# Kernel tuning notes

Hardware: AMD Instinct MI355X
Metric: run time of the kernel (lower is better)

Reference implementation:

```python
import jax, jax.numpy as jnp
import numpy as np

R = 12            # search_radius
P = 2 * R + 1     # 25x25 search window
DIV = 512.0       # self.div_num; T = DIV**-0.5


def _relu_l2norm(x, axis=1, eps=1e-12):
    # matches F.relu followed by F.normalize(p=2, dim=1)
    x = jax.nn.relu(x)
    n = jnp.sqrt(jnp.sum(x * x, axis=axis, keepdims=True))
    return x / jnp.maximum(n, eps)


def setup_inputs() -> dict:
    key = jax.random.key(0)
    k1, k2 = jax.random.split(key)
    feat1_video = jax.random.normal(k1, (8, 512, 4, 30, 30), dtype=jnp.float32)  # r50_feat1 (pre relu/norm)
    feat2_img = jax.random.normal(k2, (8, 512, 30, 30), dtype=jnp.float32)       # img_feat2 (pre relu/norm)
    return {"feat1_video": feat1_video, "feat2_img": feat2_img}


def reference(feat1_video, feat2_img):
    # relu + channel L2-normalize, as in forward() before compute_corr_softmax
    video = _relu_l2norm(feat1_video)          # [B,C,T,H,W]  -> r50_feat2 arg
    patch = _relu_l2norm(feat2_img)            # [B,C,H,W]    -> patch_feat1 arg
    B, C, T, H, W = video.shape

    vpad = jnp.pad(video, ((0, 0), (0, 0), (0, 0), (R, R), (R, R)))

    # all 625 (dh, dw) window offsets, vmapped into one fused correlation
    offsets = jnp.stack(
        jnp.meshgrid(jnp.arange(P), jnp.arange(P), indexing="ij"), axis=-1
    ).reshape(-1, 2)  # [P*P, 2]

    def shift_corr(off):
        win = jax.lax.dynamic_slice(
            vpad, (0, 0, 0, off[0], off[1]), (B, C, T, H, W)
        )
        return jnp.einsum("bcthw,bchw->bthw", win, patch)

    corr = jax.vmap(shift_corr)(offsets)               # [P*P, B, T, H, W]
    corr = jnp.transpose(corr, (1, 2, 0, 3, 4))        # [B, T, P*P, H, W]

    # torch: div by div_num**-0.5, then softmax(corr / T) with T = div_num**-0.5
    Tparam = DIV ** (-0.5)
    corr = corr / (DIV ** (-0.5)) / Tparam             # == corr * 512
    sm = jax.nn.softmax(corr, axis=2)

    # validity mask: output pixel y with shift h=dh-R is valid iff 0 <= y+h < H
    dh = jnp.arange(P)
    ys = jnp.arange(H)
    xs = jnp.arange(W)
    valid_h = ((ys[None, :] + dh[:, None] - R) >= 0) & ((ys[None, :] + dh[:, None] - R) < H)  # [P,H]
    valid_w = ((xs[None, :] + dh[:, None] - R) >= 0) & ((xs[None, :] + dh[:, None] - R) < W)  # [P,W]
    valid = valid_h[:, None, :, None] & valid_w[None, :, None, :]  # [P,P,H,W]
    valid = valid.reshape(P * P, H, W)

    out = jnp.where(valid[None, None], sm, jnp.float32(-1.0))      # [B,T,P*P,H,W]
    return out.reshape(B, T, P, P, H, W)
```

## Files before the change

kernel.cpp:

```cpp
#include <hip/hip_runtime.h>

#define RR 12
#define PD 25
#define PP 625
#define HH 30
#define WW 30
#define HWD 900
#define CD 512
#define BD 8
#define TD 4
#define CSTRIDE 628
#define ROWPKB 32768
#define QSCALE 16129.0f
#define EXPK (512.0f / QSCALE)

typedef __attribute__((ext_vector_type(4))) int i32x4;
typedef __attribute__((ext_vector_type(16))) int i32x16;

__global__ __launch_bounds__(256) void norm_pack_kernel(const float* __restrict__ inP,
                                                        const float* __restrict__ inV,
                                                        unsigned char* __restrict__ outA,
                                                        unsigned char* __restrict__ outB) {
    int row = blockIdx.x;
    int plane = blockIdx.y;
    const float* in;
    size_t base;
    int c_stride;
    unsigned char* ob;
    if (plane < 8) {
        in = inP; c_stride = HWD;
        base = (size_t)plane * CD * HWD + row * WW;
        ob = outA + (size_t)(plane * 30 + row) * ROWPKB;
    } else {
        int bt = plane - 8;
        int b = bt >> 2, t = bt & 3;
        in = inV; c_stride = TD * HWD;
        base = (size_t)b * CD * (TD * HWD) + (size_t)t * HWD + row * WW;
        ob = outB + (size_t)(bt * 30 + row) * ROWPKB;
    }
    __shared__ float tile[30][516];
    __shared__ float inv[30];
    int tid = threadIdx.x;
    for (int it = 0; it < 64; ++it) {
        int lin = it * 256 + tid;
        int c = lin >> 5, p = lin & 31;
        if (p < 30) tile[p][c] = fmaxf(in[base + (size_t)c * c_stride + p], 0.f);
    }
    __syncthreads();
    if ((tid >> 3) < 30) {
        int p = tid >> 3, s8 = tid & 7;
        float acc = 0.f;
#pragma unroll
        for (int j = 0; j < 16; ++j) {
            const float4 v = *reinterpret_cast<const float4*>(&tile[p][(s8 + j * 8) * 4]);
            acc += v.x * v.x + v.y * v.y + v.z * v.z + v.w * v.w;
        }
        acc += __shfl_xor(acc, 1);
        acc += __shfl_xor(acc, 2);
        acc += __shfl_xor(acc, 4);
        if (s8 == 0) inv[p] = 1.0f / fmaxf(sqrtf(acc), 1e-12f);
    }
    __syncthreads();
    for (int sl = tid; sl < 1024; sl += 256) {
        int ks = sl >> 6, ln = sl & 63;
        int x = ln & 31;
        if (x > 29) x = 29;
        int kb = ks * 32 + (ln >> 5) * 16;
        float iv = inv[x];
        union { signed char c[16]; i32x4 v; } p1, p2;
#pragma unroll
        for (int j = 0; j < 16; ++j) {
            float nv = tile[x][kb + j] * iv;
            float s1 = rintf(nv * 127.f);
            float r = nv * 127.f - s1;
            float s2 = rintf(r * 254.f);
            p1.c[j] = (signed char)(int)s1;
            p2.c[j] = (signed char)(int)s2;
        }
        *(i32x4*)(ob + (size_t)ks * 2048 + ln * 16) = p1.v;
        *(i32x4*)(ob + (size_t)ks * 2048 + 1024 + ln * 16) = p2.v;
    }
}

__global__ __launch_bounds__(512, 4) void corr_kernel(
    const unsigned char* __restrict__ Apk, const unsigned char* __restrict__ Bpk,
    float* __restrict__ out) {
    int gid = blockIdx.x;
    int r = gid & 7;
    int x_ = gid >> 3;
    int btl = x_ / 30;
    int h = x_ - btl * 30;
    int bt = r * 4 + btl;
    int b = r;

    __shared__ float corr[HH * CSTRIDE];
    __shared__ float is_lds[HH];
    int tid = threadIdx.x;
    int wid = tid >> 6, lane = tid & 63;

    for (int i = tid; i < HH * CSTRIDE; i += 512) corr[i] = 0.f;

    const unsigned char* abase = Apk + (size_t)(b * 30 + h) * ROWPKB + lane * 16;
    const unsigned char* bplane = Bpk + (size_t)bt * 30 * ROWPKB + lane * 16;
    int dh_lo = max(0, RR - h);
    int dh_hi = min(PD - 1, HH - 1 + RR - h);
    __syncthreads();

    for (int dh = dh_lo + wid; dh <= dh_hi; dh += 8) {
        int y = h + dh - RR;
        const unsigned char* bbase = bplane + (size_t)y * ROWPKB;
        i32x16 s11, s12, s21, s22;
#pragma unroll
        for (int i = 0; i < 16; ++i) { s11[i] = 0; s12[i] = 0; s21[i] = 0; s22[i] = 0; }
#pragma unroll 8
        for (int ks = 0; ks < 16; ++ks) {
            i32x4 a1 = *(const i32x4*)(abase + ks * 2048);
            i32x4 a2 = *(const i32x4*)(abase + ks * 2048 + 1024);
            i32x4 b1 = *(const i32x4*)(bbase + ks * 2048);
            i32x4 b2 = *(const i32x4*)(bbase + ks * 2048 + 1024);
            s11 = __builtin_amdgcn_mfma_i32_32x32x32_i8(a1, b1, s11, 0, 0, 0);
            s12 = __builtin_amdgcn_mfma_i32_32x32x32_i8(a1, b2, s12, 0, 0, 0);
            s21 = __builtin_amdgcn_mfma_i32_32x32x32_i8(a2, b1, s21, 0, 0, 0);
            s22 = __builtin_amdgcn_mfma_i32_32x32x32_i8(a2, b2, s22, 0, 0, 0);
        }
        int x = lane & 31;
        if (x < 30) {
            int rbase = 4 * (lane >> 5);
#pragma unroll
            for (int rr = 0; rr < 16; ++rr) {
                int w = (rr & 3) + 8 * (rr >> 2) + rbase;
                int dw = x - w + RR;
                if (w < 30 && (unsigned)dw < (unsigned)PD) {
                    float c = fmaf((float)(s12[rr] + s21[rr]), 1.0f / 254.0f,
                                   (float)s11[rr]) +
                              (float)s22[rr] * (1.0f / 64516.0f);
                    corr[w * CSTRIDE + dh * PD + dw] = c;
                }
            }
        }
    }
    __syncthreads();

    for (int w = wid; w < WW; w += 8) {
        float m = 0.f;
        for (int i = lane; i < PP; i += 64) m = fmaxf(m, corr[w * CSTRIDE + i]);
        m = fmaxf(m, __shfl_xor(m, 1));
        m = fmaxf(m, __shfl_xor(m, 2));
        m = fmaxf(m, __shfl_xor(m, 4));
        m = fmaxf(m, __shfl_xor(m, 8));
        m = fmaxf(m, __shfl_xor(m, 16));
        m = fmaxf(m, __shfl_xor(m, 32));
        float s = 0.f;
        for (int i = lane; i < PP; i += 64) {
            float e = __expf(EXPK * (corr[w * CSTRIDE + i] - m));
            s += e;
            corr[w * CSTRIDE + i] = e;
        }
        s += __shfl_xor(s, 1);
        s += __shfl_xor(s, 2);
        s += __shfl_xor(s, 4);
        s += __shfl_xor(s, 8);
        s += __shfl_xor(s, 16);
        s += __shfl_xor(s, 32);
        if (lane == 0) is_lds[w] = 1.0f / s;
    }
    __syncthreads();

    float* obase = out + (size_t)bt * PP * HWD + h * WW;
    for (int idx = tid; idx < PP * 32; idx += 512) {
        int w = idx & 31;
        if (w < 30) {
            int i = idx >> 5;
            int dh = i / 25, dw = i - dh * 25;
            bool valid = ((unsigned)(h + dh - RR) < (unsigned)HH) &&
                         ((unsigned)(w + dw - RR) < (unsigned)WW);
            float val = -1.0f;
            if (valid) val = corr[w * CSTRIDE + i] * is_lds[w];
            obase[(size_t)i * HWD + w] = val;
        }
    }
}

extern "C" void kernel_launch(void* const* d_in, const int* in_sizes, int n_in,
                              void* d_out, int out_size, void* d_ws, size_t ws_size,
                              hipStream_t stream) {
    const float* feat1 = (const float*)d_in[0];
    const float* feat2 = (const float*)d_in[1];
    float* out = (float*)d_out;
    unsigned char* Apk = (unsigned char*)d_ws;
    unsigned char* Bpk = Apk + (size_t)BD * 30 * ROWPKB;

    norm_pack_kernel<<<dim3(30, 40), 256, 0, stream>>>(feat2, feat1, Apk, Bpk);
    corr_kernel<<<dim3(960), 512, 0, stream>>>(Apk, Bpk, out);
}
```

Before: 126.3 us.

## Fuse online softmax stats into MFMA loop, stage A row in LDS, use 12 waves

Caches the A row in shared memory instead of reloading it from global memory for each dh. Raises the block to 12 waves, each computing a per-wave online max and sum while its MFMA results are written. The per-wave stats are then merged and the invalid zero entries are accounted for analytically. This removes the corr zero-fill and the separate max and exp pass over LDS. In exchange it adds many shuffle reductions per dh, recomputes exp at output time, and uses about 32KB more LDS, which lowers how many blocks fit per CU.

```diff
diff --git a/kernel.cpp b/kernel.cpp
--- a/kernel.cpp
+++ b/kernel.cpp
@@ -82,7 +82,7 @@
     }
 }
 
-__global__ __launch_bounds__(512, 4) void corr_kernel(
+__global__ __launch_bounds__(768, 3) void corr_kernel(
     const unsigned char* __restrict__ Apk, const unsigned char* __restrict__ Bpk,
     float* __restrict__ out) {
     int gid = blockIdx.x;
@@ -94,19 +94,34 @@
     int b = r;
 
     __shared__ float corr[HH * CSTRIDE];
+    __shared__ unsigned char alds[ROWPKB];
+    __shared__ float stats_m[12][30];
+    __shared__ float stats_s[12][30];
+    __shared__ float m_lds[HH];
     __shared__ float is_lds[HH];
     int tid = threadIdx.x;
     int wid = tid >> 6, lane = tid & 63;
 
-    for (int i = tid; i < HH * CSTRIDE; i += 512) corr[i] = 0.f;
-
-    const unsigned char* abase = Apk + (size_t)(b * 30 + h) * ROWPKB + lane * 16;
+    {
+        const uint4* src = (const uint4*)(Apk + (size_t)(b * 30 + h) * ROWPKB);
+        uint4* dst = (uint4*)alds;
+        for (int i = tid; i < 2048; i += 768) dst[i] = src[i];
+    }
     const unsigned char* bplane = Bpk + (size_t)bt * 30 * ROWPKB + lane * 16;
     int dh_lo = max(0, RR - h);
     int dh_hi = min(PD - 1, HH - 1 + RR - h);
     __syncthreads();
 
-    for (int dh = dh_lo + wid; dh <= dh_hi; dh += 8) {
+    const unsigned char* albase = alds + lane * 16;
+    float om[16], os[16];
+#pragma unroll
+    for (int i = 0; i < 16; ++i) { om[i] = -1e38f; os[i] = 0.f; }
+
+    int x = lane & 31;
+    bool xv = x < 30;
+    int rbase = 4 * (lane >> 5);
+
+    for (int dh = dh_lo + wid; dh <= dh_hi; dh += 12) {
         int y = h + dh - RR;
         const unsigned char* bbase = bplane + (size_t)y * ROWPKB;
         i32x16 s11, s12, s21, s22;
@@ -114,8 +129,8 @@
         for (int i = 0; i < 16; ++i) { s11[i] = 0; s12[i] = 0; s21[i] = 0; s22[i] = 0; }
 #pragma unroll 8
         for (int ks = 0; ks < 16; ++ks) {
-            i32x4 a1 = *(const i32x4*)(abase + ks * 2048);
-            i32x4 a2 = *(const i32x4*)(abase + ks * 2048 + 1024);
+            i32x4 a1 = *(const i32x4*)(albase + ks * 2048);
+            i32x4 a2 = *(const i32x4*)(albase + ks * 2048 + 1024);
             i32x4 b1 = *(const i32x4*)(bbase + ks * 2048);
             i32x4 b2 = *(const i32x4*)(bbase + ks * 2048 + 1024);
             s11 = __builtin_amdgcn_mfma_i32_32x32x32_i8(a1, b1, s11, 0, 0, 0);
@@ -123,51 +138,65 @@
             s21 = __builtin_amdgcn_mfma_i32_32x32x32_i8(a2, b1, s21, 0, 0, 0);
             s22 = __builtin_amdgcn_mfma_i32_32x32x32_i8(a2, b2, s22, 0, 0, 0);
         }
-        int x = lane & 31;
-        if (x < 30) {
-            int rbase = 4 * (lane >> 5);
-#pragma unroll
-            for (int rr = 0; rr < 16; ++rr) {
-                int w = (rr & 3) + 8 * (rr >> 2) + rbase;
-                int dw = x - w + RR;
-                if (w < 30 && (unsigned)dw < (unsigned)PD) {
-                    float c = fmaf((float)(s12[rr] + s21[rr]), 1.0f / 254.0f,
-                                   (float)s11[rr]) +
-                              (float)s22[rr] * (1.0f / 64516.0f);
-                    corr[w * CSTRIDE + dh * PD + dw] = c;
-                }
-            }
-        }
-    }
-    __syncthreads();
-
-    for (int w = wid; w < WW; w += 8) {
-        float m = 0.f;
-        for (int i = lane; i < PP; i += 64) m = fmaxf(m, corr[w * CSTRIDE + i]);
-        m = fmaxf(m, __shfl_xor(m, 1));
-        m = fmaxf(m, __shfl_xor(m, 2));
-        m = fmaxf(m, __shfl_xor(m, 4));
-        m = fmaxf(m, __shfl_xor(m, 8));
-        m = fmaxf(m, __shfl_xor(m, 16));
-        m = fmaxf(m, __shfl_xor(m, 32));
-        float s = 0.f;
-        for (int i = lane; i < PP; i += 64) {
-            float e = __expf(EXPK * (corr[w * CSTRIDE + i] - m));
-            s += e;
-            corr[w * CSTRIDE + i] = e;
-        }
-        s += __shfl_xor(s, 1);
-        s += __shfl_xor(s, 2);
-        s += __shfl_xor(s, 4);
-        s += __shfl_xor(s, 8);
-        s += __shfl_xor(s, 16);
-        s += __shfl_xor(s, 32);
-        if (lane == 0) is_lds[w] = 1.0f / s;
+#pragma unroll
+        for (int rr = 0; rr < 16; ++rr) {
+            int w = (rr & 3) + 8 * (rr >> 2) + rbase;
+            float c = fmaf((float)(s12[rr] + s21[rr]), 1.0f / 254.0f,
+                           (float)s11[rr]) +
+                      (float)s22[rr] * (1.0f / 64516.0f);
+            int dw = x - w + RR;
+            bool valid = xv && ((unsigned)dw < (unsigned)PD) && (w < 30);
+            if (valid) corr[w * CSTRIDE + dh * PD + dw] = c;
+            float cv = valid ? c : -1e38f;
+            float lm = cv;
+            lm = fmaxf(lm, __shfl_xor(lm, 1));
+            lm = fmaxf(lm, __shfl_xor(lm, 2));
+            lm = fmaxf(lm, __shfl_xor(lm, 4));
+            lm = fmaxf(lm, __shfl_xor(lm, 8));
+            lm = fmaxf(lm, __shfl_xor(lm, 16));
+            float nm = fmaxf(om[rr], lm);
+            float e = __expf(EXPK * (cv - nm));
+            float ls = e;
+            ls += __shfl_xor(ls, 1);
+            ls += __shfl_xor(ls, 2);
+            ls += __shfl_xor(ls, 4);
+            ls += __shfl_xor(ls, 8);
+            ls += __shfl_xor(ls, 16);
+            os[rr] = fmaf(os[rr], __expf(EXPK * (om[rr] - nm)), ls);
+            om[rr] = nm;
+        }
+    }
+
+    if (lane == 0 || lane == 32) {
+#pragma unroll
+        for (int rr = 0; rr < 16; ++rr) {
+            int w = (rr & 3) + 8 * (rr >> 2) + rbase;
+            if (w < 30) { stats_m[wid][w] = om[rr]; stats_s[wid][w] = os[rr]; }
+        }
+    }
+    __syncthreads();
+
+    if (tid < 30) {
+        int w = tid;
+        float mstar = -1e38f;
+#pragma unroll
+        for (int i = 0; i < 12; ++i) mstar = fmaxf(mstar, stats_m[i][w]);
+        float ss = 0.f;
+#pragma unroll
+        for (int i = 0; i < 12; ++i)
+            ss += stats_s[i][w] * __expf(EXPK * (stats_m[i][w] - mstar));
+        int lo_w = max(0, RR - w), hi_w = min(PD - 1, WW - 1 + RR - w);
+        int nvw = hi_w - lo_w + 1;
+        int nvh = dh_hi - dh_lo + 1;
+        float zeros = (float)(PP - nvh * nvw);
+        ss += zeros * __expf(-EXPK * mstar);
+        m_lds[w] = mstar;
+        is_lds[w] = 1.0f / ss;
     }
     __syncthreads();
 
     float* obase = out + (size_t)bt * PP * HWD + h * WW;
-    for (int idx = tid; idx < PP * 32; idx += 512) {
+    for (int idx = tid; idx < PP * 32; idx += 768) {
         int w = idx & 31;
         if (w < 30) {
             int i = idx >> 5;
@@ -175,7 +204,8 @@
             bool valid = ((unsigned)(h + dh - RR) < (unsigned)HH) &&
                          ((unsigned)(w + dw - RR) < (unsigned)WW);
             float val = -1.0f;
-            if (valid) val = corr[w * CSTRIDE + i] * is_lds[w];
+            if (valid)
+                val = __expf(EXPK * (corr[w * CSTRIDE + i] - m_lds[w])) * is_lds[w];
             obase[(size_t)i * HWD + w] = val;
         }
     }
@@ -191,5 +221,5 @@
     unsigned char* Bpk = Apk + (size_t)BD * 30 * ROWPKB;
 
     norm_pack_kernel<<<dim3(30, 40), 256, 0, stream>>>(feat2, feat1, Apk, Bpk);
-    corr_kernel<<<dim3(960), 512, 0, stream>>>(Apk, Bpk, out);
+    corr_kernel<<<dim3(960), 768, 0, stream>>>(Apk, Bpk, out);
 }
```

New measurement: 154.8 us. +22.6%, slower.
